# Kernel tuning notes

Hardware: AMD Instinct MI355X
Metric: run time of the kernel (lower is better)

## Reference

```python
import jax, jax.numpy as jnp
import numpy as np

N, K, C = 65536, 4096, 64  # batch_dim, num_codes, num_channels


def setup_inputs() -> dict:
    key = jax.random.key(0)
    k1, k2 = jax.random.split(key)
    keys = jax.random.normal(k1, (N, C), dtype=jnp.float32)
    # GlorotNormal-scaled codebook, as in the original layer init
    scale = jnp.sqrt(2.0 / (K + C)).astype(jnp.float32)
    embeddings = jax.random.normal(k2, (K, C), dtype=jnp.float32) * scale
    return {"keys": keys, "embeddings": embeddings}


def reference(keys, embeddings):
    # logits: negative squared euclidean distance to each code, [N, K]
    logits = (2.0 * (keys @ embeddings.T)
              - jnp.sum(keys * keys, axis=-1, keepdims=True)
              - jnp.sum(embeddings * embeddings, axis=-1))
    # training=True path: categorical sample via Gumbel-max (fixed key -> deterministic)
    gumbel = jax.random.gumbel(jax.random.key(1), logits.shape, dtype=logits.dtype)
    idx = jnp.argmax(logits + gumbel, axis=-1)           # [N] int
    quantized = embeddings[idx]                           # gather, [N, C]
    # straight-through: forward value = quantized, gradient flows to keys
    samples = keys + jax.lax.stop_gradient(quantized - keys)
    log_probs = jax.nn.log_softmax(logits, axis=-1)
    return samples, log_probs
```

## Files before the change

### kernel.cpp

```cpp
#include <hip/hip_runtime.h>
#include <hip/hip_bf16.h>
#include <stdint.h>


#define NROWS 65536
#define KCODES 4096
#define NPAIR 32768
#define LP_OFF 4194304ull

#define WS_T 0u
#define WS_S 65536u
#define WS_LSE 327680u
#define WS_E16 589824u
#define WS_B 1114112u
#define WS_PB 2686976u

typedef float f32x4_t __attribute__((ext_vector_type(4)));
typedef short s16x8_t __attribute__((ext_vector_type(8)));

__device__ __forceinline__ uint32_t rotl32(uint32_t x, int r) {
  return (x << r) | (x >> (32 - r));
}

__device__ __forceinline__ void threefry(uint32_t x0, uint32_t x1,
                                         uint32_t& o0, uint32_t& o1) {
  const uint32_t k0 = 0u, k1 = 1u, k2 = 0x1BD11BDBu;
  x0 += k0; x1 += k1;
  x0 += x1; x1 = rotl32(x1, 13); x1 ^= x0;
  x0 += x1; x1 = rotl32(x1, 15); x1 ^= x0;
  x0 += x1; x1 = rotl32(x1, 26); x1 ^= x0;
  x0 += x1; x1 = rotl32(x1, 6);  x1 ^= x0;
  x0 += k1; x1 += k2 + 1u;
  x0 += x1; x1 = rotl32(x1, 17); x1 ^= x0;
  x0 += x1; x1 = rotl32(x1, 29); x1 ^= x0;
  x0 += x1; x1 = rotl32(x1, 16); x1 ^= x0;
  x0 += x1; x1 = rotl32(x1, 24); x1 ^= x0;
  x0 += k2; x1 += k0 + 2u;
  x0 += x1; x1 = rotl32(x1, 13); x1 ^= x0;
  x0 += x1; x1 = rotl32(x1, 15); x1 ^= x0;
  x0 += x1; x1 = rotl32(x1, 26); x1 ^= x0;
  x0 += x1; x1 = rotl32(x1, 6);  x1 ^= x0;
  x0 += k0; x1 += k1 + 3u;
  x0 += x1; x1 = rotl32(x1, 17); x1 ^= x0;
  x0 += x1; x1 = rotl32(x1, 29); x1 ^= x0;
  x0 += x1; x1 = rotl32(x1, 16); x1 ^= x0;
  x0 += x1; x1 = rotl32(x1, 24); x1 ^= x0;
  x0 += k1; x1 += k2 + 4u;
  x0 += x1; x1 = rotl32(x1, 13); x1 ^= x0;
  x0 += x1; x1 = rotl32(x1, 15); x1 ^= x0;
  x0 += x1; x1 = rotl32(x1, 26); x1 ^= x0;
  x0 += x1; x1 = rotl32(x1, 6);  x1 ^= x0;
  x0 += k2; x1 += k0 + 5u;
  o0 = x0; o1 = x1;
}

__device__ __forceinline__ float hw_log(float x) {
  float r;
  asm("v_log_f32 %0, %1" : "=v"(r) : "v"(x));
  return __fmul_rn(r, 0.69314718056f);
}

__device__ __forceinline__ float gumbel_bits(uint32_t b) {
  float f = __fsub_rn(__uint_as_float(0x3f800000u | (b >> 9)), 1.0f);
  float u = fmaxf(f, 1.17549435e-38f);
  float w = -hw_log(u);
  return -hw_log(w);
}

__device__ __forceinline__ unsigned short f2bf(float x) {
  uint32_t u = __float_as_uint(x);
  uint32_t r = (u + 0x7fffu + ((u >> 16) & 1u)) >> 16;
  return (unsigned short)r;
}
__device__ __forceinline__ float bf2f(unsigned short u) {
  return __uint_as_float((uint32_t)u << 16);
}

__global__ void vq_pre(const float* __restrict__ emb, float* __restrict__ t_ws,
                       unsigned short* __restrict__ e16,
                       unsigned short* __restrict__ wsb) {
  int code = blockIdx.x * 256 + threadIdx.x;
  if (code >= KCODES) return;
  const float* e = emb + (size_t)code * 64;
  float v[64];
#pragma unroll
  for (int i = 0; i < 64; ++i) v[i] = e[i];
  float r[8];
#pragma unroll
  for (int j = 0; j < 8; ++j) r[j] = __fmul_rn(v[j], v[j]);
#pragma unroll
  for (int m = 1; m < 8; ++m)
#pragma unroll
    for (int j = 0; j < 8; ++j) r[j] = __fadd_rn(r[j], __fmul_rn(v[m * 8 + j], v[m * 8 + j]));
  t_ws[code] = __fadd_rn(__fadd_rn(__fadd_rn(r[0], r[1]), __fadd_rn(r[2], r[3])),
                         __fadd_rn(__fadd_rn(r[4], r[5]), __fadd_rn(r[6], r[7])));
  const int ct = code >> 4, col = code & 15;
#pragma unroll
  for (int h = 0; h < 2; ++h) {
#pragma unroll
    for (int kg = 0; kg < 4; ++kg) {
      s16x8_t c0, c1, c2;
#pragma unroll
      for (int j = 0; j < 8; ++j) {
        float x = v[h * 32 + kg * 8 + j];
        unsigned short b0 = f2bf(x);
        float r1 = __fsub_rn(x, bf2f(b0));
        unsigned short b1 = f2bf(r1);
        float r2 = __fsub_rn(r1, bf2f(b1));
        unsigned short b2 = f2bf(r2);
        c0[j] = (short)b0; c1[j] = (short)b1; c2[j] = (short)b2;
      }
      *(s16x8_t*)(e16 + (size_t)code * 64 + h * 32 + kg * 8) = c0;
      size_t base = ((size_t)(ct * 6 + h) * 64 + kg * 16 + col) * 8;
      *(s16x8_t*)(wsb + base) = c0;
      *(s16x8_t*)(wsb + base + (size_t)2 * 64 * 8) = c1;
      *(s16x8_t*)(wsb + base + (size_t)4 * 64 * 8) = c2;
    }
  }
}

__global__ void vq_prek(const float* __restrict__ keys, float* __restrict__ s_ws) {
  int row = blockIdx.x * 256 + threadIdx.x;
  const float* p = keys + (size_t)row * 64;
  float v[64];
#pragma unroll
  for (int i = 0; i < 64; ++i) v[i] = p[i];
  float r[8];
#pragma unroll
  for (int j = 0; j < 8; ++j) r[j] = __fmul_rn(v[j], v[j]);
#pragma unroll
  for (int m = 1; m < 8; ++m)
#pragma unroll
    for (int j = 0; j < 8; ++j) r[j] = __fadd_rn(r[j], __fmul_rn(v[m * 8 + j], v[m * 8 + j]));
  s_ws[row] = __fadd_rn(__fadd_rn(__fadd_rn(r[0], r[1]), __fadd_rn(r[2], r[3])),
                        __fadd_rn(__fadd_rn(r[4], r[5]), __fadd_rn(r[6], r[7])));
}

__global__ __launch_bounds__(256) void vq_lse(const float* __restrict__ keys,
                                              const unsigned short* __restrict__ e16,
                                              const float* __restrict__ t_ws,
                                              float* __restrict__ lse_ws) {
  const int tid = threadIdx.x;
  const int w = tid >> 6, lane = tid & 63;
  const int r0 = blockIdx.x * 64 + w * 16;
  const int mrow = lane & 15, kg = lane >> 4;

  const float* ka = keys + (size_t)(r0 + mrow) * 64 + kg * 8;
  float av[16];
#pragma unroll
  for (int i = 0; i < 8; ++i) av[i] = ka[i];
#pragma unroll
  for (int i = 0; i < 8; ++i) av[8 + i] = ka[32 + i];
  float sp = 0.f;
#pragma unroll
  for (int i = 0; i < 16; ++i) sp = fmaf(av[i], av[i], sp);
  sp += __shfl_xor(sp, 16);
  sp += __shfl_xor(sp, 32);

  s16x8_t a0, a1;
#pragma unroll
  for (int i = 0; i < 8; ++i) { a0[i] = (short)f2bf(av[i]); a1[i] = (short)f2bf(av[8 + i]); }

  float S0 = 0.f, S1 = 0.f, S2 = 0.f, S3 = 0.f;
  for (int ct = 0; ct < 256; ++ct) {
    const int col = ct * 16 + mrow;
    const s16x8_t b0 = *(const s16x8_t*)(e16 + (size_t)col * 64 + kg * 8);
    const s16x8_t b1 = *(const s16x8_t*)(e16 + (size_t)col * 64 + 32 + kg * 8);
    f32x4_t acc = {0.f, 0.f, 0.f, 0.f};
    acc = __builtin_amdgcn_mfma_f32_16x16x32_bf16(a0, b0, acc, 0, 0, 0);
    acc = __builtin_amdgcn_mfma_f32_16x16x32_bf16(a1, b1, acc, 0, 0, 0);
    const float tc = t_ws[col];
    S0 += __expf(2.f * acc[0] - tc);
    S1 += __expf(2.f * acc[1] - tc);
    S2 += __expf(2.f * acc[2] - tc);
    S3 += __expf(2.f * acc[3] - tc);
  }
#pragma unroll
  for (int m = 1; m <= 8; m <<= 1) {
    S0 += __shfl_xor(S0, m); S1 += __shfl_xor(S1, m);
    S2 += __shfl_xor(S2, m); S3 += __shfl_xor(S3, m);
  }
  float s0 = __shfl(sp, kg * 4 + 0);
  float s1 = __shfl(sp, kg * 4 + 1);
  float s2 = __shfl(sp, kg * 4 + 2);
  float s3 = __shfl(sp, kg * 4 + 3);
  if (mrow == 0) {
    lse_ws[r0 + kg * 4 + 0] = logf(S0) - s0;
    lse_ws[r0 + kg * 4 + 1] = logf(S1) - s1;
    lse_ws[r0 + kg * 4 + 2] = logf(S2) - s2;
    lse_ws[r0 + kg * 4 + 3] = logf(S3) - s3;
  }
}

#define TERM(sa, sb)                                                             \
  accL = __builtin_amdgcn_mfma_f32_16x16x32_bf16(aL[sa][0], B[(sb)*2+0], accL, 0, 0, 0); \
  accH = __builtin_amdgcn_mfma_f32_16x16x32_bf16(aH[sa][0], B[(sb)*2+0], accH, 0, 0, 0); \
  accL = __builtin_amdgcn_mfma_f32_16x16x32_bf16(aL[sa][1], B[(sb)*2+1], accL, 0, 0, 0); \
  accH = __builtin_amdgcn_mfma_f32_16x16x32_bf16(aH[sa][1], B[(sb)*2+1], accH, 0, 0, 0);

__global__ __launch_bounds__(256, 3) void vq_main2(
    const float* __restrict__ keys, const float* __restrict__ emb,
    const float* __restrict__ t_ws, const float* __restrict__ s_ws,
    const float* __restrict__ lse_ws, const unsigned short* __restrict__ wsb,
    float2* __restrict__ pb_ws, float* __restrict__ out) {
  const int tid = threadIdx.x;
  const int lane = tid & 63;
  const int wv = blockIdx.x * 4 + (tid >> 6);
  const int grp = wv >> 1;
  const int half = wv & 1;
  const int ct0 = half * 128;
  const int r16 = lane & 15;
  const int kg = lane >> 4;
  const int nlo = grp * 16, nhi = nlo + NPAIR;

  s16x8_t aL[3][2], aH[3][2];
  {
    const float* pL = keys + (size_t)(nlo + r16) * 64 + kg * 8;
    const float* pH = keys + (size_t)(nhi + r16) * 64 + kg * 8;
#pragma unroll
    for (int h = 0; h < 2; ++h) {
#pragma unroll
      for (int j = 0; j < 8; ++j) {
        float x = pL[h * 32 + j];
        unsigned short b0 = f2bf(x);
        float r1 = __fsub_rn(x, bf2f(b0));
        unsigned short b1 = f2bf(r1);
        float r2 = __fsub_rn(r1, bf2f(b1));
        aL[0][h][j] = (short)b0; aL[1][h][j] = (short)b1; aL[2][h][j] = (short)f2bf(r2);
        x = pH[h * 32 + j];
        b0 = f2bf(x); r1 = __fsub_rn(x, bf2f(b0)); b1 = f2bf(r1);
        r2 = __fsub_rn(r1, bf2f(b1));
        aH[0][h][j] = (short)b0; aH[1][h][j] = (short)b1; aH[2][h][j] = (short)f2bf(r2);
      }
    }
  }

  float sL[4], sH[4], lseL[4], lseH[4];
  uint32_t obL[4], obH[4];
#pragma unroll
  for (int r = 0; r < 4; ++r) {
    sL[r] = s_ws[nlo + kg * 4 + r];
    sH[r] = s_ws[nhi + kg * 4 + r];
    lseL[r] = lse_ws[nlo + kg * 4 + r];
    lseH[r] = lse_ws[nhi + kg * 4 + r];
    obL[r] = (uint32_t)(nlo + kg * 4 + r) * 4096u + (uint32_t)r16;
    obH[r] = (uint32_t)(nhi + kg * 4 + r) * 4096u + (uint32_t)r16;
  }

  float bestL[4], bestH[4];
  int biL[4], biH[4];
#pragma unroll
  for (int r = 0; r < 4; ++r) {
    bestL[r] = bestH[r] = -__builtin_inff();
    biL[r] = biH[r] = 0;
  }

  float* outLP = out + LP_OFF;
  const s16x8_t* bp = (const s16x8_t*)wsb + (size_t)ct0 * 6 * 64 + lane;

  s16x8_t B[6];
#pragma unroll
  for (int f = 0; f < 6; ++f) B[f] = bp[f * 64];

  for (int ct = ct0; ct < ct0 + 128; ++ct) {
    f32x4_t accL = {0.f, 0.f, 0.f, 0.f}, accH = {0.f, 0.f, 0.f, 0.f};
    TERM(1, 1) TERM(2, 0) TERM(0, 2) TERM(1, 0) TERM(0, 1) TERM(0, 0)

    const float tk = t_ws[ct * 16 + r16];
    if (ct < ct0 + 127) {
      bp += 6 * 64;
#pragma unroll
      for (int f = 0; f < 6; ++f) B[f] = bp[f * 64];
    }

#pragma unroll
    for (int r = 0; r < 4; ++r) {
      const uint32_t j = obL[r] + (uint32_t)(ct * 16);
      uint32_t o0, o1;
      threefry(j, j + 0x08000000u, o0, o1);
      const float lL = __fsub_rn(__fsub_rn(__fmul_rn(2.0f, accL[r]), sL[r]), tk);
      const float lH = __fsub_rn(__fsub_rn(__fmul_rn(2.0f, accH[r]), sH[r]), tk);
      const float vL = __fadd_rn(lL, gumbel_bits(o0));
      const float vH = __fadd_rn(lH, gumbel_bits(o1));
      const int k = ct * 16 + r16;
      if (vL > bestL[r]) { bestL[r] = vL; biL[r] = k; }
      if (vH > bestH[r]) { bestH[r] = vH; biH[r] = k; }
      outLP[(size_t)obL[r] + (size_t)(ct * 16)] = __fsub_rn(lL, lseL[r]);
      outLP[(size_t)obH[r] + (size_t)(ct * 16)] = __fsub_rn(lH, lseH[r]);
    }
  }

#pragma unroll
  for (int r = 0; r < 4; ++r) {
#pragma unroll
    for (int m = 1; m <= 8; m <<= 1) {
      float ov = __shfl_xor(bestL[r], m);
      int oi = __shfl_xor(biL[r], m);
      if (ov > bestL[r] || (ov == bestL[r] && oi < biL[r])) { bestL[r] = ov; biL[r] = oi; }
      ov = __shfl_xor(bestH[r], m);
      oi = __shfl_xor(biH[r], m);
      if (ov > bestH[r] || (ov == bestH[r] && oi < biH[r])) { bestH[r] = ov; biH[r] = oi; }
    }
  }

  if (r16 == 0) {
#pragma unroll
    for (int r = 0; r < 4; ++r) {
      pb_ws[(size_t)(nlo + kg * 4 + r) * 2 + half] =
          make_float2(bestL[r], __int_as_float(biL[r]));
      pb_ws[(size_t)(nhi + kg * 4 + r) * 2 + half] =
          make_float2(bestH[r], __int_as_float(biH[r]));
    }
  }
}

__global__ __launch_bounds__(256) void vq_fin(const float* __restrict__ keys,
                                              const float* __restrict__ emb,
                                              const float2* __restrict__ pb_ws,
                                              float* __restrict__ out) {
  const int t = blockIdx.x * 256 + threadIdx.x;
  const int row = t >> 4, l16 = t & 15;
  const float2 a = pb_ws[(size_t)row * 2 + 0];
  const float2 b = pb_ws[(size_t)row * 2 + 1];
  const int bi = (b.x > a.x) ? __float_as_int(b.y) : __float_as_int(a.y);
  const float4 qq = *(const float4*)(emb + (size_t)bi * 64 + l16 * 4);
  const float4 kv = *(const float4*)(keys + (size_t)row * 64 + l16 * 4);
  float4 rr;
  rr.x = __fadd_rn(kv.x, __fsub_rn(qq.x, kv.x));
  rr.y = __fadd_rn(kv.y, __fsub_rn(qq.y, kv.y));
  rr.z = __fadd_rn(kv.z, __fsub_rn(qq.z, kv.z));
  rr.w = __fadd_rn(kv.w, __fsub_rn(qq.w, kv.w));
  *(float4*)(out + (size_t)row * 64 + l16 * 4) = rr;
}

extern "C" void kernel_launch(void* const* d_in, const int* in_sizes, int n_in,
                              void* d_out, int out_size, void* d_ws, size_t ws_size,
                              hipStream_t stream) {
  const float* keys = (const float*)d_in[0];
  const float* emb = (const float*)d_in[1];
  float* out = (float*)d_out;
  char* w = (char*)d_ws;
  float* t_ws = (float*)(w + WS_T);
  float* s_ws = (float*)(w + WS_S);
  float* lse_ws = (float*)(w + WS_LSE);
  unsigned short* e16 = (unsigned short*)(w + WS_E16);
  unsigned short* wsb = (unsigned short*)(w + WS_B);
  float2* pb_ws = (float2*)(w + WS_PB);

  vq_pre<<<16, 256, 0, stream>>>(emb, t_ws, e16, wsb);
  vq_prek<<<256, 256, 0, stream>>>(keys, s_ws);
  vq_lse<<<1024, 256, 0, stream>>>(keys, e16, t_ws, lse_ws);
  vq_main2<<<1024, 256, 0, stream>>>(keys, emb, t_ws, s_ws, lse_ws, wsb, pb_ws, out);
  vq_fin<<<4096, 256, 0, stream>>>(keys, emb, pb_ws, out);
}
```

Measured before the change: 801.7 us.

## Split LSE pass across code quarters with paired row tiles and reduce partials

Each wave in the log-sum-exp pass now handles two 16-row tiles (a low and a high half of the batch) that share every codebook fragment load, and covers only a quarter of the codes. The per-quarter partial sums go to a new workspace buffer, and a small extra kernel adds them and applies the log and row-norm correction. This is meant to halve codebook reads per MFMA and to launch more, shorter waves for better occupancy. In exchange it adds a kernel launch and a partial-sum round trip through memory, and row norms now come from the separate prek buffer instead of being recomputed.

```diff
diff --git a/kernel.cpp b/kernel.cpp
--- a/kernel.cpp
+++ b/kernel.cpp
@@ -14,6 +14,7 @@
 #define WS_E16 589824u
 #define WS_B 1114112u
 #define WS_PB 2686976u
+#define WS_PS 3735552u
 
 typedef float f32x4_t __attribute__((ext_vector_type(4)));
 typedef short s16x8_t __attribute__((ext_vector_type(8)));
@@ -136,60 +137,78 @@
                         __fadd_rn(__fadd_rn(r[4], r[5]), __fadd_rn(r[6], r[7])));
 }
 
-__global__ __launch_bounds__(256) void vq_lse(const float* __restrict__ keys,
-                                              const unsigned short* __restrict__ e16,
-                                              const float* __restrict__ t_ws,
-                                              float* __restrict__ lse_ws) {
+__global__ __launch_bounds__(256, 6) void vq_lsep(
+    const float* __restrict__ keys, const unsigned short* __restrict__ e16,
+    const float* __restrict__ t_ws, float* __restrict__ pS) {
   const int tid = threadIdx.x;
-  const int w = tid >> 6, lane = tid & 63;
-  const int r0 = blockIdx.x * 64 + w * 16;
+  const int lane = tid & 63;
+  const int wv = blockIdx.x * 4 + (tid >> 6);
+  const int grp = wv >> 2;
+  const int qt = wv & 3;
   const int mrow = lane & 15, kg = lane >> 4;
-
-  const float* ka = keys + (size_t)(r0 + mrow) * 64 + kg * 8;
-  float av[16];
-#pragma unroll
-  for (int i = 0; i < 8; ++i) av[i] = ka[i];
-#pragma unroll
-  for (int i = 0; i < 8; ++i) av[8 + i] = ka[32 + i];
-  float sp = 0.f;
-#pragma unroll
-  for (int i = 0; i < 16; ++i) sp = fmaf(av[i], av[i], sp);
-  sp += __shfl_xor(sp, 16);
-  sp += __shfl_xor(sp, 32);
-
-  s16x8_t a0, a1;
-#pragma unroll
-  for (int i = 0; i < 8; ++i) { a0[i] = (short)f2bf(av[i]); a1[i] = (short)f2bf(av[8 + i]); }
-
-  float S0 = 0.f, S1 = 0.f, S2 = 0.f, S3 = 0.f;
-  for (int ct = 0; ct < 256; ++ct) {
+  const int nlo = grp * 16, nhi = nlo + NPAIR;
+
+  s16x8_t aL0, aL1, aH0, aH1;
+  {
+    const float* pL = keys + (size_t)(nlo + mrow) * 64 + kg * 8;
+    const float* pH = keys + (size_t)(nhi + mrow) * 64 + kg * 8;
+#pragma unroll
+    for (int j = 0; j < 8; ++j) {
+      aL0[j] = (short)f2bf(pL[j]);
+      aL1[j] = (short)f2bf(pL[32 + j]);
+      aH0[j] = (short)f2bf(pH[j]);
+      aH1[j] = (short)f2bf(pH[32 + j]);
+    }
+  }
+
+  float SL0 = 0.f, SL1 = 0.f, SL2 = 0.f, SL3 = 0.f;
+  float SH0 = 0.f, SH1 = 0.f, SH2 = 0.f, SH3 = 0.f;
+
+  for (int ct = qt * 64; ct < qt * 64 + 64; ++ct) {
     const int col = ct * 16 + mrow;
     const s16x8_t b0 = *(const s16x8_t*)(e16 + (size_t)col * 64 + kg * 8);
     const s16x8_t b1 = *(const s16x8_t*)(e16 + (size_t)col * 64 + 32 + kg * 8);
-    f32x4_t acc = {0.f, 0.f, 0.f, 0.f};
-    acc = __builtin_amdgcn_mfma_f32_16x16x32_bf16(a0, b0, acc, 0, 0, 0);
-    acc = __builtin_amdgcn_mfma_f32_16x16x32_bf16(a1, b1, acc, 0, 0, 0);
+    f32x4_t accL = {0.f, 0.f, 0.f, 0.f}, accH = {0.f, 0.f, 0.f, 0.f};
+    accL = __builtin_amdgcn_mfma_f32_16x16x32_bf16(aL0, b0, accL, 0, 0, 0);
+    accH = __builtin_amdgcn_mfma_f32_16x16x32_bf16(aH0, b0, accH, 0, 0, 0);
+    accL = __builtin_amdgcn_mfma_f32_16x16x32_bf16(aL1, b1, accL, 0, 0, 0);
+    accH = __builtin_amdgcn_mfma_f32_16x16x32_bf16(aH1, b1, accH, 0, 0, 0);
     const float tc = t_ws[col];
-    S0 += __expf(2.f * acc[0] - tc);
-    S1 += __expf(2.f * acc[1] - tc);
-    S2 += __expf(2.f * acc[2] - tc);
-    S3 += __expf(2.f * acc[3] - tc);
+    SL0 += __expf(2.f * accL[0] - tc);
+    SL1 += __expf(2.f * accL[1] - tc);
+    SL2 += __expf(2.f * accL[2] - tc);
+    SL3 += __expf(2.f * accL[3] - tc);
+    SH0 += __expf(2.f * accH[0] - tc);
+    SH1 += __expf(2.f * accH[1] - tc);
+    SH2 += __expf(2.f * accH[2] - tc);
+    SH3 += __expf(2.f * accH[3] - tc);
   }
 #pragma unroll
   for (int m = 1; m <= 8; m <<= 1) {
-    S0 += __shfl_xor(S0, m); S1 += __shfl_xor(S1, m);
-    S2 += __shfl_xor(S2, m); S3 += __shfl_xor(S3, m);
-  }
-  float s0 = __shfl(sp, kg * 4 + 0);
-  float s1 = __shfl(sp, kg * 4 + 1);
-  float s2 = __shfl(sp, kg * 4 + 2);
-  float s3 = __shfl(sp, kg * 4 + 3);
+    SL0 += __shfl_xor(SL0, m); SL1 += __shfl_xor(SL1, m);
+    SL2 += __shfl_xor(SL2, m); SL3 += __shfl_xor(SL3, m);
+    SH0 += __shfl_xor(SH0, m); SH1 += __shfl_xor(SH1, m);
+    SH2 += __shfl_xor(SH2, m); SH3 += __shfl_xor(SH3, m);
+  }
   if (mrow == 0) {
-    lse_ws[r0 + kg * 4 + 0] = logf(S0) - s0;
-    lse_ws[r0 + kg * 4 + 1] = logf(S1) - s1;
-    lse_ws[r0 + kg * 4 + 2] = logf(S2) - s2;
-    lse_ws[r0 + kg * 4 + 3] = logf(S3) - s3;
-  }
+    pS[(size_t)(nlo + kg * 4 + 0) * 4 + qt] = SL0;
+    pS[(size_t)(nlo + kg * 4 + 1) * 4 + qt] = SL1;
+    pS[(size_t)(nlo + kg * 4 + 2) * 4 + qt] = SL2;
+    pS[(size_t)(nlo + kg * 4 + 3) * 4 + qt] = SL3;
+    pS[(size_t)(nhi + kg * 4 + 0) * 4 + qt] = SH0;
+    pS[(size_t)(nhi + kg * 4 + 1) * 4 + qt] = SH1;
+    pS[(size_t)(nhi + kg * 4 + 2) * 4 + qt] = SH2;
+    pS[(size_t)(nhi + kg * 4 + 3) * 4 + qt] = SH3;
+  }
+}
+
+__global__ __launch_bounds__(256) void vq_lsefin(const float* __restrict__ pS,
+                                                 const float* __restrict__ s_ws,
+                                                 float* __restrict__ lse_ws) {
+  const int row = blockIdx.x * 256 + threadIdx.x;
+  const float4 q = *(const float4*)(pS + (size_t)row * 4);
+  const float S = (q.x + q.y) + (q.z + q.w);
+  lse_ws[row] = logf(S) - s_ws[row];
 }
 
 #define TERM(sa, sb)                                                             \
@@ -346,10 +365,12 @@
   unsigned short* e16 = (unsigned short*)(w + WS_E16);
   unsigned short* wsb = (unsigned short*)(w + WS_B);
   float2* pb_ws = (float2*)(w + WS_PB);
+  float* pS_ws = (float*)(w + WS_PS);
 
   vq_pre<<<16, 256, 0, stream>>>(emb, t_ws, e16, wsb);
   vq_prek<<<256, 256, 0, stream>>>(keys, s_ws);
-  vq_lse<<<1024, 256, 0, stream>>>(keys, e16, t_ws, lse_ws);
+  vq_lsep<<<2048, 256, 0, stream>>>(keys, e16, t_ws, pS_ws);
+  vq_lsefin<<<256, 256, 0, stream>>>(pS_ws, s_ws, lse_ws);
   vq_main2<<<1024, 256, 0, stream>>>(keys, emb, t_ws, s_ws, lse_ws, wsb, pb_ws, out);
   vq_fin<<<4096, 256, 0, stream>>>(keys, emb, pb_ws, out);
 }
```

New measurement: 699.9 us. 12.7% less time.
